# Kernel optimization log

Measured on AMD Instinct MI355X. Metric: run time of the kernel, lower is better.

## Reference

```python
import jax, jax.numpy as jnp
import numpy as np

C = 512
CI = C // 4  # inter_channels
EPS = 1e-5


def _conv1x1(x, w, b):
    # x: [B,C,H,W], w: [O,C], b: [O] -> [B,O,H,W]
    return jnp.einsum('bchw,oc->bohw', x, w) + b[None, :, None, None]


def _maxpool2(t):
    # 2x2 max pool, stride 2 (NCHW)
    b, c, h, w = t.shape
    return t.reshape(b, c, h // 2, 2, w // 2, 2).max(axis=(3, 5))


def setup_inputs() -> dict:
    key = jax.random.key(0)
    ks = jax.random.split(key, 9)
    B, H, W = 8, 64, 64
    s_in = 1.0 / np.sqrt(C)
    s_ci = 1.0 / np.sqrt(CI)
    return {
        'x': jax.random.normal(ks[0], (B, C, H, W), jnp.float32),
        'g_w': jax.random.normal(ks[1], (CI, C), jnp.float32) * s_in,
        'g_b': jnp.zeros((CI,), jnp.float32),
        'phi_w': jax.random.normal(ks[2], (CI, C), jnp.float32) * s_in,
        'phi_b': jnp.zeros((CI,), jnp.float32),
        'theta_w': jax.random.normal(ks[3], (CI, C), jnp.float32) * s_in,
        'theta_b': jnp.zeros((CI,), jnp.float32),
        'W_w': jax.random.normal(ks[4], (C, CI), jnp.float32) * s_ci,
        'W_b': jnp.zeros((C,), jnp.float32),
        'ln_gamma': jax.random.normal(ks[5], (C,), jnp.float32) * 0.02 + 1.0,
        'ln_beta': jnp.zeros((C,), jnp.float32),
    }


def reference(x, g_w, g_b, phi_w, phi_b, theta_w, theta_b, W_w, W_b, ln_gamma, ln_beta):
    B, Cc, H, Wd = x.shape
    N = H * Wd
    # projections; g and phi are maxpool-downsampled (N/4 key/value positions)
    g_x = _maxpool2(_conv1x1(x, g_w, g_b)).reshape(B, CI, N // 4)          # [B,Ci,M]
    phi_x = _maxpool2(_conv1x1(x, phi_w, phi_b)).reshape(B, CI, N // 4)    # [B,Ci,M]
    theta_x = _conv1x1(x, theta_w, theta_b).reshape(B, CI, N)              # [B,Ci,N]
    # attention: QK^T -> softmax -> V
    f = jnp.einsum('bcn,bcm->bnm', theta_x, phi_x)                          # [B,N,M]
    attn = jax.nn.softmax(f, axis=-1)
    y = jnp.einsum('bnm,bcm->bcn', attn, g_x).reshape(B, CI, H, Wd)         # [B,Ci,H,W]
    # output projection + channels-first LayerNorm + residual
    W_y = _conv1x1(y, W_w, W_b)                                             # [B,C,H,W]
    mu = W_y.mean(axis=1, keepdims=True)
    var = W_y.var(axis=1, keepdims=True)
    W_y = (W_y - mu) * jax.lax.rsqrt(var + EPS)
    W_y = W_y * ln_gamma[None, :, None, None] + ln_beta[None, :, None, None]
    return W_y + x
```

## Files before the change

kernel.cpp:

```cpp
#include <hip/hip_runtime.h>
#include <math.h>

constexpr int Cc  = 512;
constexpr int CIc = 128;
constexpr int Bc  = 8;
constexpr int Nc  = 4096;
constexpr int Mc  = 1024;

typedef __bf16 bf16x8 __attribute__((ext_vector_type(8)));
typedef float  f32x4  __attribute__((ext_vector_type(4)));

__device__ __forceinline__ unsigned short f2bf(float f) {
  unsigned u = __float_as_uint(f);
  u += 0x7fffu + ((u >> 16) & 1u);
  return (unsigned short)(u >> 16);
}
__device__ __forceinline__ float bf2f(unsigned short h) {
  return __uint_as_float((unsigned)h << 16);
}
__device__ __forceinline__ unsigned pack2bf(float lo, float hi) {
  return (unsigned)f2bf(lo) | ((unsigned)f2bf(hi) << 16);
}

__device__ __forceinline__ void gload16(const void* g, void* lds) {
  __builtin_amdgcn_global_load_lds(
      (const __attribute__((address_space(1))) unsigned int*)g,
      (__attribute__((address_space(3))) unsigned int*)lds, 16, 0, 0);
}

__global__ __launch_bounds__(256) void k_prep(
    const float* __restrict__ gw, const float* __restrict__ pw,
    const float* __restrict__ tw, const float* __restrict__ Ww,
    const float* __restrict__ gb, const float* __restrict__ pb,
    const float* __restrict__ tb,
    unsigned short* __restrict__ wcat, unsigned short* __restrict__ wwb,
    float* __restrict__ bcat) {
  int i = blockIdx.x * 256 + threadIdx.x;
  if (i < 49152) {
    int c = i >> 7, q = i & 127;
    const float* src = (c < 128) ? tw + (size_t)c * 512
                     : (c < 256) ? pw + (size_t)(c - 128) * 512
                                 : gw + (size_t)(c - 256) * 512;
    float4 v = *(const float4*)(src + q * 4);
    ushort4 o;
    o.x = f2bf(v.x); o.y = f2bf(v.y); o.z = f2bf(v.z); o.w = f2bf(v.w);
    *(ushort4*)(wcat + (size_t)c * 512 + q * 4) = o;
  } else if (i < 65536) {
    int i2 = i - 49152;
    int c = i2 >> 5, q = i2 & 31;
    float4 v = *(const float4*)(Ww + (size_t)c * 128 + q * 4);
    ushort4 o;
    o.x = f2bf(v.x); o.y = f2bf(v.y); o.z = f2bf(v.z); o.w = f2bf(v.w);
    *(ushort4*)(wwb + (size_t)c * 128 + q * 4) = o;
  } else if (i < 65920) {
    int j = i - 65536;
    bcat[j] = (j < 128) ? tb[j] : (j < 256) ? pb[j - 128] : gb[j - 256];
  }
}

__global__ __launch_bounds__(512) void k_conv_all(
    const float* __restrict__ x, const unsigned short* __restrict__ wcat,
    const float* __restrict__ bcat,
    unsigned short* __restrict__ theta_t, unsigned short* __restrict__ phi_t,
    unsigned short* __restrict__ gbuf) {
  __shared__ __align__(16) char smem[98304];
  const int b = blockIdx.y, h2 = blockIdx.x, n0 = h2 * 128;
  const int t = threadIdx.x;
  const int w = t >> 6, l = t & 63, lr = l & 15, lg = l >> 4;

  const char* wsrc = (const char*)wcat;
  int woff[6];
#pragma unroll
  for (int i = 0; i < 6; ++i) {
    int r = (w * 6 + i) * 8 + (l >> 3);
    woff[i] = r * 1024 + (((l & 7) * 16) ^ ((r & 7) << 4));
  }

  const float* xb = x + (size_t)b * Cc * Nc + n0 + w * 16 + lr;

  float xraw[16];
#define LOADX(k0_)                                                        \
  {                                                                       \
    _Pragma("unroll")                                                     \
    for (int ks = 0; ks < 2; ++ks)                                        \
      _Pragma("unroll")                                                   \
      for (int j = 0; j < 8; ++j)                                         \
        xraw[ks * 8 + j] = xb[(size_t)((k0_) + ks * 32 + lg * 8 + j) * Nc]; \
  }
#define STAGEW(buf_, k0_)                                                 \
  {                                                                       \
    char* dst_ = smem + (buf_) * 49152;                                   \
    _Pragma("unroll")                                                     \
    for (int i = 0; i < 6; ++i)                                           \
      gload16(wsrc + (size_t)(k0_) * 2 + woff[i], dst_ + (w * 6 + i) * 1024); \
  }

  f32x4 acc[24];
#pragma unroll
  for (int tc = 0; tc < 24; ++tc) acc[tc] = (f32x4){0.f, 0.f, 0.f, 0.f};

  LOADX(0);
  STAGEW(0, 0);
  asm volatile("s_waitcnt vmcnt(0)" ::: "memory");
  __builtin_amdgcn_s_barrier();

  for (int c = 0; c < 8; ++c) {
    const int cur = c & 1;
    bf16x8 af[2];
#pragma unroll
    for (int ks = 0; ks < 2; ++ks) {
      union { unsigned u[4]; bf16x8 v; } ab;
#pragma unroll
      for (int q = 0; q < 4; ++q)
        ab.u[q] = pack2bf(xraw[ks * 8 + 2 * q], xraw[ks * 8 + 2 * q + 1]);
      af[ks] = ab.v;
    }
    if (c < 7) {
      LOADX((c + 1) * 64);
      STAGEW(cur ^ 1, (c + 1) * 64);
    }
    const char* Wb = smem + cur * 49152;
    __builtin_amdgcn_s_setprio(1);
#pragma unroll
    for (int ks = 0; ks < 2; ++ks)
#pragma unroll
      for (int tc = 0; tc < 24; ++tc) {
        int r = tc * 16 + lr;
        bf16x8 bfr = *(const bf16x8*)(
            Wb + r * 128 + ((lg * 16 + ks * 64) ^ ((lr & 7) << 4)));
        acc[tc] = __builtin_amdgcn_mfma_f32_16x16x32_bf16(af[ks], bfr, acc[tc], 0, 0, 0);
      }
    __builtin_amdgcn_s_setprio(0);
    asm volatile("s_waitcnt vmcnt(0)" ::: "memory");
    __builtin_amdgcn_s_barrier();
  }
#undef LOADX
#undef STAGEW

  unsigned short* PG = (unsigned short*)smem;
  unsigned short* Yt = (unsigned short*)(smem + 67584);
  const int rbase = w * 16 + lg * 4;

#pragma unroll
  for (int tc = 8; tc < 24; ++tc) {
    float bv = bcat[tc * 16 + lr];
#pragma unroll
    for (int reg = 0; reg < 4; ++reg)
      PG[(rbase + reg) * 264 + tc * 16 + lr - 128] = f2bf(acc[tc][reg] + bv);
  }
  if (w < 4) {
#pragma unroll
    for (int tc = 0; tc < 8; ++tc) {
      float bv = bcat[tc * 16 + lr];
#pragma unroll
      for (int reg = 0; reg < 4; ++reg)
        Yt[(rbase + reg) * 136 + tc * 16 + lr] = f2bf(acc[tc][reg] + bv);
    }
  }
  __syncthreads();
#pragma unroll
  for (int it = 0; it < 2; ++it) {
    int idx = it * 512 + t, n = idx >> 4, j = idx & 15;
    *(bf16x8*)(theta_t + (((size_t)(b * Nc + n0 + n)) << 7) + j * 8) =
        *(const bf16x8*)(Yt + n * 136 + j * 8);
  }
  {
    int mloc = t >> 4, j = t & 15;
    const unsigned short* r0 = &PG[(2 * mloc) * 264 + j * 8];
    const unsigned short* r1 = &PG[(2 * mloc + 1) * 264 + j * 8];
    const unsigned short* r2 = &PG[(64 + 2 * mloc) * 264 + j * 8];
    const unsigned short* r3 = &PG[(65 + 2 * mloc) * 264 + j * 8];
    unsigned short o[8];
#pragma unroll
    for (int q = 0; q < 8; ++q)
      o[q] = f2bf(fmaxf(fmaxf(bf2f(r0[q]), bf2f(r1[q])),
                        fmaxf(bf2f(r2[q]), bf2f(r3[q]))));
    unsigned short* dp = phi_t + (((size_t)(b * Mc + h2 * 32 + mloc)) << 7) + j * 8;
    *(ushort4*)dp = *(ushort4*)o;
    *(ushort4*)(dp + 4) = *(ushort4*)(o + 4);
  }
  {
    int ci = t >> 2, mq = t & 3;
    unsigned short tmp[8];
#pragma unroll
    for (int q = 0; q < 8; ++q) {
      int w2 = mq * 8 + q;
      float m0 = fmaxf(
          fmaxf(bf2f(PG[(2 * w2) * 264 + 128 + ci]),
                bf2f(PG[(2 * w2 + 1) * 264 + 128 + ci])),
          fmaxf(bf2f(PG[(64 + 2 * w2) * 264 + 128 + ci]),
                bf2f(PG[(65 + 2 * w2) * 264 + 128 + ci])));
      tmp[q] = f2bf(m0);
    }
    unsigned short* dst = gbuf + ((size_t)(b * CIc + ci)) * Mc + h2 * 32 + mq * 8;
    *(ushort4*)(dst) = *(ushort4*)(tmp);
    *(ushort4*)(dst + 4) = *(ushort4*)(tmp + 4);
  }
  __syncthreads();
  if (w >= 4) {
#pragma unroll
    for (int tc = 0; tc < 8; ++tc) {
      float bv = bcat[tc * 16 + lr];
#pragma unroll
      for (int reg = 0; reg < 4; ++reg)
        Yt[((w - 4) * 16 + lg * 4 + reg) * 136 + tc * 16 + lr] =
            f2bf(acc[tc][reg] + bv);
    }
  }
  __syncthreads();
#pragma unroll
  for (int it = 0; it < 2; ++it) {
    int idx = it * 512 + t, n = idx >> 4, j = idx & 15;
    *(bf16x8*)(theta_t + (((size_t)(b * Nc + n0 + 64 + n)) << 7) + j * 8) =
        *(const bf16x8*)(Yt + n * 136 + j * 8);
  }
}

__global__ __launch_bounds__(256) void k_attn_mfma(
    const unsigned short* __restrict__ theta_t,
    const unsigned short* __restrict__ phi_t,
    const unsigned short* __restrict__ gv,
    unsigned short* __restrict__ y_t) {
  __shared__ __align__(16) char Kb[2][16384];
  __shared__ __align__(16) char Vb[2][16384];
  __shared__ __align__(16) unsigned short Ps[4][16][72];
  const int b = blockIdx.y, n0 = blockIdx.x * 64;
  const int tid = threadIdx.x;
  const int w = tid >> 6, l = tid & 63;
  const int lr = l & 15, lg = l >> 4;

  const int krow_l = l >> 4, kchunk = (l & 15) * 16;
  const int vrow_l = l >> 3, vchunk = (l & 7) * 16;
  int koff[4], voff[4];
#pragma unroll
  for (int i = 0; i < 4; ++i) {
    int kr = w * 16 + i * 4 + krow_l;
    koff[i] = kr * 256 + (kchunk ^ ((kr & 7) << 4));
    int vr = w * 32 + i * 8 + vrow_l;
    voff[i] = vr * 2048 + (vchunk ^ ((vr & 7) << 4));
  }
  const char* kbase = (const char*)(phi_t + (((size_t)(b * Mc)) << 7));
  const char* vbase = (const char*)(gv + (((size_t)b) << 17));

  auto stage = [&](int buf, int t) {
#pragma unroll
    for (int i = 0; i < 4; ++i)
      gload16(kbase + t * 16384 + koff[i], &Kb[buf][(w * 4 + i) * 1024]);
#pragma unroll
    for (int i = 0; i < 4; ++i)
      gload16(vbase + t * 128 + voff[i], &Vb[buf][(w * 4 + i) * 1024]);
  };

  bf16x8 qf[4];
  {
    const unsigned short* qp =
        theta_t + (((size_t)(b * Nc + n0 + w * 16 + lr)) << 7);
#pragma unroll
    for (int kk = 0; kk < 4; ++kk)
      qf[kk] = *(const bf16x8*)(qp + kk * 32 + lg * 8);
  }
  f32x4 of[8];
#pragma unroll
  for (int ct = 0; ct < 8; ++ct) of[ct] = (f32x4){0.f, 0.f, 0.f, 0.f};
  float run_m[4], run_l[4];
#pragma unroll
  for (int r = 0; r < 4; ++r) { run_m[r] = -1e30f; run_l[r] = 0.f; }

  stage(0, 0);
  asm volatile("s_waitcnt vmcnt(0)" ::: "memory");
  __builtin_amdgcn_s_barrier();

  for (int t = 0; t < Mc / 64; ++t) {
    const int cur = t & 1;
    if (t + 1 < Mc / 64) stage(cur ^ 1, t + 1);
    const char* Ks = Kb[cur];
    const char* Vs = Vb[cur];
    f32x4 sm[4];
    __builtin_amdgcn_s_setprio(1);
#pragma unroll
    for (int mt = 0; mt < 4; ++mt) {
      f32x4 s = (f32x4){0.f, 0.f, 0.f, 0.f};
#pragma unroll
      for (int kk = 0; kk < 4; ++kk) {
        bf16x8 kf = *(const bf16x8*)(
            Ks + (mt * 16 + lr) * 256 + ((kk * 64 + lg * 16) ^ ((lr & 7) << 4)));
        s = __builtin_amdgcn_mfma_f32_16x16x32_bf16(qf[kk], kf, s, 0, 0, 0);
      }
      sm[mt] = s;
    }
    __builtin_amdgcn_s_setprio(0);
    float pmax[4];
#pragma unroll
    for (int reg = 0; reg < 4; ++reg) {
      float mx = fmaxf(fmaxf(sm[0][reg], sm[1][reg]), fmaxf(sm[2][reg], sm[3][reg]));
      mx = fmaxf(mx, __shfl_xor(mx, 1));
      mx = fmaxf(mx, __shfl_xor(mx, 2));
      mx = fmaxf(mx, __shfl_xor(mx, 4));
      mx = fmaxf(mx, __shfl_xor(mx, 8));
      pmax[reg] = mx;
    }
    bool need = (pmax[0] > run_m[0] + 8.f) | (pmax[1] > run_m[1] + 8.f) |
                (pmax[2] > run_m[2] + 8.f) | (pmax[3] > run_m[3] + 8.f);
    if (__any(need)) {
#pragma unroll
      for (int reg = 0; reg < 4; ++reg) {
        float nm = fmaxf(run_m[reg], pmax[reg]);
        float sc = __expf(run_m[reg] - nm);
        run_m[reg] = nm;
        run_l[reg] *= sc;
#pragma unroll
        for (int ct = 0; ct < 8; ++ct) of[ct][reg] *= sc;
      }
    }
#pragma unroll
    for (int reg = 0; reg < 4; ++reg) {
      float p0 = __expf(sm[0][reg] - run_m[reg]);
      float p1 = __expf(sm[1][reg] - run_m[reg]);
      float p2 = __expf(sm[2][reg] - run_m[reg]);
      float p3 = __expf(sm[3][reg] - run_m[reg]);
      unsigned pk01, pk23;
      asm("v_cvt_pk_bf16_f32 %0, %1, %2" : "=v"(pk01) : "v"(p0), "v"(p1));
      asm("v_cvt_pk_bf16_f32 %0, %1, %2" : "=v"(pk23) : "v"(p2), "v"(p3));
      unsigned short* pr = &Ps[w][lg * 4 + reg][lr];
      pr[0]  = (unsigned short)pk01;
      pr[16] = (unsigned short)(pk01 >> 16);
      pr[32] = (unsigned short)pk23;
      pr[48] = (unsigned short)(pk23 >> 16);
      float rs = (p0 + p1) + (p2 + p3);
      rs += __shfl_xor(rs, 1);
      rs += __shfl_xor(rs, 2);
      rs += __shfl_xor(rs, 4);
      rs += __shfl_xor(rs, 8);
      run_l[reg] += rs;
    }
    bf16x8 pa0 = *(const bf16x8*)(&Ps[w][lr][lg * 8]);
    bf16x8 pa1 = *(const bf16x8*)(&Ps[w][lr][32 + lg * 8]);
    __builtin_amdgcn_s_setprio(1);
#pragma unroll
    for (int ct = 0; ct < 8; ++ct) {
      bf16x8 vf0 = *(const bf16x8*)(
          Vs + (ct * 16 + lr) * 128 + ((lg * 16) ^ ((lr & 7) << 4)));
      of[ct] = __builtin_amdgcn_mfma_f32_16x16x32_bf16(pa0, vf0, of[ct], 0, 0, 0);
      bf16x8 vf1 = *(const bf16x8*)(
          Vs + (ct * 16 + lr) * 128 + ((64 + lg * 16) ^ ((lr & 7) << 4)));
      of[ct] = __builtin_amdgcn_mfma_f32_16x16x32_bf16(pa1, vf1, of[ct], 0, 0, 0);
    }
    __builtin_amdgcn_s_setprio(0);
    asm volatile("s_waitcnt vmcnt(0)" ::: "memory");
    __builtin_amdgcn_s_barrier();
  }
  float invl[4];
#pragma unroll
  for (int reg = 0; reg < 4; ++reg) invl[reg] = 1.f / run_l[reg];
  unsigned short* Ys = (unsigned short*)Kb;
#pragma unroll
  for (int ct = 0; ct < 8; ++ct)
#pragma unroll
    for (int reg = 0; reg < 4; ++reg)
      Ys[(w * 16 + lg * 4 + reg) * 128 + ct * 16 + lr] =
          f2bf(of[ct][reg] * invl[reg]);
  __syncthreads();
#pragma unroll
  for (int it = 0; it < 4; ++it) {
    int i = it * 256 + tid;
    int r = i >> 4, cl = i & 15;
    *(bf16x8*)(y_t + (((size_t)(b * Nc + n0 + r)) << 7) + cl * 8) =
        *(const bf16x8*)(Ys + r * 128 + cl * 8);
  }
}

__global__ __launch_bounds__(256) void k_wconv_mfma(
    const unsigned short* __restrict__ y_t, const unsigned short* __restrict__ wwb,
    const float* __restrict__ wbias, const float* __restrict__ gamma,
    const float* __restrict__ beta, const float* __restrict__ x,
    float* __restrict__ out) {
  __shared__ __align__(16) char smem[36864];
  unsigned short* WTs = (unsigned short*)smem;
  float* Ys = (float*)smem;
  const int b = blockIdx.y, n0 = blockIdx.x * 64;
  const int t = threadIdx.x;
  const int w = t >> 6, l = t & 63, lr = l & 15, lg = l >> 4;

  bf16x8 qf[4];
  {
    const unsigned short* qp = y_t + (((size_t)(b * Nc + n0 + w * 16 + lr)) << 7);
#pragma unroll
    for (int kk = 0; kk < 4; ++kk)
      qf[kk] = *(const bf16x8*)(qp + kk * 32 + lg * 8);
  }
  f32x4 acc[32];
#pragma unroll
  for (int i = 0; i < 32; ++i) acc[i] = (f32x4){0.f, 0.f, 0.f, 0.f};

#pragma unroll
  for (int cc = 0; cc < 4; ++cc) {
    __syncthreads();
#pragma unroll
    for (int it = 0; it < 8; ++it) {
      int i = it * 256 + t;
      int r = i >> 4, j = i & 15;
      bf16x8 v = *(const bf16x8*)(wwb + (((size_t)(cc * 128 + r)) << 7) + j * 8);
      *(bf16x8*)((char*)WTs + r * 256 + ((j * 16) ^ ((r & 7) << 4))) = v;
    }
    __syncthreads();
#pragma unroll
    for (int tc = 0; tc < 8; ++tc) {
      f32x4 a = acc[cc * 8 + tc];
      int r = tc * 16 + lr;
#pragma unroll
      for (int kk = 0; kk < 4; ++kk) {
        bf16x8 kf = *(const bf16x8*)(
            (char*)WTs + r * 256 + ((kk * 64 + lg * 16) ^ ((lr & 7) << 4)));
        a = __builtin_amdgcn_mfma_f32_16x16x32_bf16(qf[kk], kf, a, 0, 0, 0);
      }
      acc[cc * 8 + tc] = a;
    }
  }
  float s[4] = {0.f, 0.f, 0.f, 0.f}, q[4] = {0.f, 0.f, 0.f, 0.f};
#pragma unroll
  for (int cc = 0; cc < 4; ++cc)
#pragma unroll
    for (int tc = 0; tc < 8; ++tc) {
      float wb = wbias[cc * 128 + tc * 16 + lr];
      f32x4 a = acc[cc * 8 + tc];
#pragma unroll
      for (int reg = 0; reg < 4; ++reg) {
        a[reg] += wb;
        s[reg] += a[reg];
        q[reg] += a[reg] * a[reg];
      }
      acc[cc * 8 + tc] = a;
    }
  float mu[4], rs[4];
#pragma unroll
  for (int reg = 0; reg < 4; ++reg) {
    float sv = s[reg], qv = q[reg];
    sv += __shfl_xor(sv, 1); qv += __shfl_xor(qv, 1);
    sv += __shfl_xor(sv, 2); qv += __shfl_xor(qv, 2);
    sv += __shfl_xor(sv, 4); qv += __shfl_xor(qv, 4);
    sv += __shfl_xor(sv, 8); qv += __shfl_xor(qv, 8);
    mu[reg] = sv * (1.f / 512.f);
    float var = qv * (1.f / 512.f) - mu[reg] * mu[reg];
    rs[reg] = rsqrtf(var + 1e-5f);
  }
#pragma unroll
  for (int cc = 0; cc < 4; ++cc) {
    __syncthreads();
#pragma unroll
    for (int tc = 0; tc < 8; ++tc) {
      int c = cc * 128 + tc * 16 + lr;
      float ga = gamma[c], be = beta[c];
#pragma unroll
      for (int reg = 0; reg < 4; ++reg)
        Ys[(tc * 16 + lr) * 72 + w * 16 + lg * 4 + reg] =
            (acc[cc * 8 + tc][reg] - mu[reg]) * rs[reg] * ga + be;
    }
    __syncthreads();
#pragma unroll
    for (int it = 0; it < 8; ++it) {
      int idx = it * 256 + t;
      int r = idx >> 4, j = idx & 15;
      float4 v = *(const float4*)&Ys[r * 72 + j * 4];
      size_t gaddr = ((size_t)b * Cc + cc * 128 + r) * Nc + n0 + j * 4;
      float4 xv = *(const float4*)&x[gaddr];
      float4 o;
      o.x = v.x + xv.x; o.y = v.y + xv.y; o.z = v.z + xv.z; o.w = v.w + xv.w;
      *(float4*)&out[gaddr] = o;
    }
  }
}

extern "C" void kernel_launch(void* const* d_in, const int* in_sizes, int n_in,
                              void* d_out, int out_size, void* d_ws, size_t ws_size,
                              hipStream_t stream) {
  const float* x       = (const float*)d_in[0];
  const float* g_w     = (const float*)d_in[1];
  const float* g_b     = (const float*)d_in[2];
  const float* phi_w   = (const float*)d_in[3];
  const float* phi_b   = (const float*)d_in[4];
  const float* theta_w = (const float*)d_in[5];
  const float* theta_b = (const float*)d_in[6];
  const float* W_w     = (const float*)d_in[7];
  const float* W_b     = (const float*)d_in[8];
  const float* ln_g    = (const float*)d_in[9];
  const float* ln_b    = (const float*)d_in[10];
  float* out = (float*)d_out;

  unsigned short* theta_t = (unsigned short*)d_ws;
  unsigned short* y_t     = theta_t + (size_t)Bc * Nc * CIc;
  unsigned short* phi_t   = y_t + (size_t)Bc * Nc * CIc;
  unsigned short* gbuf    = phi_t + (size_t)Bc * Mc * CIc;
  unsigned short* wcat    = gbuf + (size_t)Bc * Mc * CIc;
  unsigned short* wwb     = wcat + (size_t)384 * 512;
  float*          bcat    = (float*)(wwb + (size_t)512 * 128);

  k_prep<<<dim3(258), dim3(256), 0, stream>>>(
      g_w, phi_w, theta_w, W_w, g_b, phi_b, theta_b, wcat, wwb, bcat);
  k_conv_all<<<dim3(Nc / 128, Bc), dim3(512), 0, stream>>>(
      x, wcat, bcat, theta_t, phi_t, gbuf);
  k_attn_mfma<<<dim3(Nc / 64, Bc), dim3(256), 0, stream>>>(
      theta_t, phi_t, gbuf, y_t);
  k_wconv_mfma<<<dim3(Nc / 64, Bc), dim3(256), 0, stream>>>(
      y_t, wwb, W_b, ln_g, ln_b, x, out);
}
```

Measured before the change: 112.6 us.

## Process two query tiles per wave in attention kernel with 128-thread blocks

Restructures the flash-attention kernel so each wave handles 32 query rows (two 16-row subtiles) instead of 16, halving the waves per block to two. Each K and V fragment read from LDS now feeds two MFMAs, which halves LDS read traffic per FLOP and gives more independent MFMA chains. The cost is roughly double the accumulator registers per wave and fewer waves per block to hide latency, which could cut occupancy.

```diff
diff --git a/kernel.cpp b/kernel.cpp
--- a/kernel.cpp
+++ b/kernel.cpp
@@ -216,55 +216,59 @@
   }
 }
 
-__global__ __launch_bounds__(256) void k_attn_mfma(
+__global__ __launch_bounds__(128) void k_attn_mfma(
     const unsigned short* __restrict__ theta_t,
     const unsigned short* __restrict__ phi_t,
     const unsigned short* __restrict__ gv,
     unsigned short* __restrict__ y_t) {
   __shared__ __align__(16) char Kb[2][16384];
   __shared__ __align__(16) char Vb[2][16384];
-  __shared__ __align__(16) unsigned short Ps[4][16][72];
+  __shared__ __align__(16) unsigned short Ps[2][32][72];
   const int b = blockIdx.y, n0 = blockIdx.x * 64;
   const int tid = threadIdx.x;
   const int w = tid >> 6, l = tid & 63;
   const int lr = l & 15, lg = l >> 4;
 
-  const int krow_l = l >> 4, kchunk = (l & 15) * 16;
-  const int vrow_l = l >> 3, vchunk = (l & 7) * 16;
-  int koff[4], voff[4];
-#pragma unroll
-  for (int i = 0; i < 4; ++i) {
-    int kr = w * 16 + i * 4 + krow_l;
-    koff[i] = kr * 256 + (kchunk ^ ((kr & 7) << 4));
-    int vr = w * 32 + i * 8 + vrow_l;
-    voff[i] = vr * 2048 + (vchunk ^ ((vr & 7) << 4));
+  int koff[8], voff[8];
+#pragma unroll
+  for (int i = 0; i < 8; ++i) {
+    int c = w * 8 + i;
+    int kr = c * 4 + (l >> 4);
+    koff[i] = kr * 256 + (((l & 15) * 16) ^ ((kr & 7) << 4));
+    int vr = c * 8 + (l >> 3);
+    voff[i] = vr * 2048 + (((l & 7) * 16) ^ ((vr & 7) << 4));
   }
   const char* kbase = (const char*)(phi_t + (((size_t)(b * Mc)) << 7));
   const char* vbase = (const char*)(gv + (((size_t)b) << 17));
 
   auto stage = [&](int buf, int t) {
 #pragma unroll
-    for (int i = 0; i < 4; ++i)
-      gload16(kbase + t * 16384 + koff[i], &Kb[buf][(w * 4 + i) * 1024]);
-#pragma unroll
-    for (int i = 0; i < 4; ++i)
-      gload16(vbase + t * 128 + voff[i], &Vb[buf][(w * 4 + i) * 1024]);
+    for (int i = 0; i < 8; ++i)
+      gload16(kbase + t * 16384 + koff[i], &Kb[buf][(w * 8 + i) * 1024]);
+#pragma unroll
+    for (int i = 0; i < 8; ++i)
+      gload16(vbase + t * 128 + voff[i], &Vb[buf][(w * 8 + i) * 1024]);
   };
 
-  bf16x8 qf[4];
-  {
+  bf16x8 qf[2][4];
+#pragma unroll
+  for (int s = 0; s < 2; ++s) {
     const unsigned short* qp =
-        theta_t + (((size_t)(b * Nc + n0 + w * 16 + lr)) << 7);
+        theta_t + (((size_t)(b * Nc + n0 + w * 32 + s * 16 + lr)) << 7);
 #pragma unroll
     for (int kk = 0; kk < 4; ++kk)
-      qf[kk] = *(const bf16x8*)(qp + kk * 32 + lg * 8);
-  }
-  f32x4 of[8];
-#pragma unroll
-  for (int ct = 0; ct < 8; ++ct) of[ct] = (f32x4){0.f, 0.f, 0.f, 0.f};
-  float run_m[4], run_l[4];
-#pragma unroll
-  for (int r = 0; r < 4; ++r) { run_m[r] = -1e30f; run_l[r] = 0.f; }
+      qf[s][kk] = *(const bf16x8*)(qp + kk * 32 + lg * 8);
+  }
+  f32x4 of[2][8];
+#pragma unroll
+  for (int s = 0; s < 2; ++s)
+#pragma unroll
+    for (int ct = 0; ct < 8; ++ct) of[s][ct] = (f32x4){0.f, 0.f, 0.f, 0.f};
+  float run_m[2][4], run_l[2][4];
+#pragma unroll
+  for (int s = 0; s < 2; ++s)
+#pragma unroll
+    for (int r = 0; r < 4; ++r) { run_m[s][r] = -1e30f; run_l[s][r] = 0.f; }
 
   stage(0, 0);
   asm volatile("s_waitcnt vmcnt(0)" ::: "memory");
@@ -275,94 +279,116 @@
     if (t + 1 < Mc / 64) stage(cur ^ 1, t + 1);
     const char* Ks = Kb[cur];
     const char* Vs = Vb[cur];
-    f32x4 sm[4];
+    f32x4 sm[2][4];
     __builtin_amdgcn_s_setprio(1);
 #pragma unroll
     for (int mt = 0; mt < 4; ++mt) {
-      f32x4 s = (f32x4){0.f, 0.f, 0.f, 0.f};
+      f32x4 s0 = (f32x4){0.f, 0.f, 0.f, 0.f};
+      f32x4 s1 = (f32x4){0.f, 0.f, 0.f, 0.f};
 #pragma unroll
       for (int kk = 0; kk < 4; ++kk) {
         bf16x8 kf = *(const bf16x8*)(
             Ks + (mt * 16 + lr) * 256 + ((kk * 64 + lg * 16) ^ ((lr & 7) << 4)));
-        s = __builtin_amdgcn_mfma_f32_16x16x32_bf16(qf[kk], kf, s, 0, 0, 0);
+        s0 = __builtin_amdgcn_mfma_f32_16x16x32_bf16(qf[0][kk], kf, s0, 0, 0, 0);
+        s1 = __builtin_amdgcn_mfma_f32_16x16x32_bf16(qf[1][kk], kf, s1, 0, 0, 0);
       }
-      sm[mt] = s;
+      sm[0][mt] = s0;
+      sm[1][mt] = s1;
     }
     __builtin_amdgcn_s_setprio(0);
-    float pmax[4];
-#pragma unroll
-    for (int reg = 0; reg < 4; ++reg) {
-      float mx = fmaxf(fmaxf(sm[0][reg], sm[1][reg]), fmaxf(sm[2][reg], sm[3][reg]));
-      mx = fmaxf(mx, __shfl_xor(mx, 1));
-      mx = fmaxf(mx, __shfl_xor(mx, 2));
-      mx = fmaxf(mx, __shfl_xor(mx, 4));
-      mx = fmaxf(mx, __shfl_xor(mx, 8));
-      pmax[reg] = mx;
-    }
-    bool need = (pmax[0] > run_m[0] + 8.f) | (pmax[1] > run_m[1] + 8.f) |
-                (pmax[2] > run_m[2] + 8.f) | (pmax[3] > run_m[3] + 8.f);
+    float pmax[2][4];
+#pragma unroll
+    for (int s = 0; s < 2; ++s)
+#pragma unroll
+      for (int reg = 0; reg < 4; ++reg) {
+        float mx = fmaxf(fmaxf(sm[s][0][reg], sm[s][1][reg]),
+                         fmaxf(sm[s][2][reg], sm[s][3][reg]));
+        mx = fmaxf(mx, __shfl_xor(mx, 1));
+        mx = fmaxf(mx, __shfl_xor(mx, 2));
+        mx = fmaxf(mx, __shfl_xor(mx, 4));
+        mx = fmaxf(mx, __shfl_xor(mx, 8));
+        pmax[s][reg] = mx;
+      }
+    bool need = false;
+#pragma unroll
+    for (int s = 0; s < 2; ++s)
+#pragma unroll
+      for (int reg = 0; reg < 4; ++reg)
+        need |= (pmax[s][reg] > run_m[s][reg] + 8.f);
     if (__any(need)) {
 #pragma unroll
+      for (int s = 0; s < 2; ++s)
+#pragma unroll
+        for (int reg = 0; reg < 4; ++reg) {
+          float nm = fmaxf(run_m[s][reg], pmax[s][reg]);
+          float sc = __expf(run_m[s][reg] - nm);
+          run_m[s][reg] = nm;
+          run_l[s][reg] *= sc;
+#pragma unroll
+          for (int ct = 0; ct < 8; ++ct) of[s][ct][reg] *= sc;
+        }
+    }
+#pragma unroll
+    for (int s = 0; s < 2; ++s)
+#pragma unroll
       for (int reg = 0; reg < 4; ++reg) {
-        float nm = fmaxf(run_m[reg], pmax[reg]);
-        float sc = __expf(run_m[reg] - nm);
-        run_m[reg] = nm;
-        run_l[reg] *= sc;
-#pragma unroll
-        for (int ct = 0; ct < 8; ++ct) of[ct][reg] *= sc;
+        float p0 = __expf(sm[s][0][reg] - run_m[s][reg]);
+        float p1 = __expf(sm[s][1][reg] - run_m[s][reg]);
+        float p2 = __expf(sm[s][2][reg] - run_m[s][reg]);
+        float p3 = __expf(sm[s][3][reg] - run_m[s][reg]);
+        unsigned pk01, pk23;
+        asm("v_cvt_pk_bf16_f32 %0, %1, %2" : "=v"(pk01) : "v"(p0), "v"(p1));
+        asm("v_cvt_pk_bf16_f32 %0, %1, %2" : "=v"(pk23) : "v"(p2), "v"(p3));
+        unsigned short* pr = &Ps[w][s * 16 + lg * 4 + reg][lr];
+        pr[0]  = (unsigned short)pk01;
+        pr[16] = (unsigned short)(pk01 >> 16);
+        pr[32] = (unsigned short)pk23;
+        pr[48] = (unsigned short)(pk23 >> 16);
+        float rs = (p0 + p1) + (p2 + p3);
+        rs += __shfl_xor(rs, 1);
+        rs += __shfl_xor(rs, 2);
+        rs += __shfl_xor(rs, 4);
+        rs += __shfl_xor(rs, 8);
+        run_l[s][reg] += rs;
       }
-    }
-#pragma unroll
-    for (int reg = 0; reg < 4; ++reg) {
-      float p0 = __expf(sm[0][reg] - run_m[reg]);
-      float p1 = __expf(sm[1][reg] - run_m[reg]);
-      float p2 = __expf(sm[2][reg] - run_m[reg]);
-      float p3 = __expf(sm[3][reg] - run_m[reg]);
-      unsigned pk01, pk23;
-      asm("v_cvt_pk_bf16_f32 %0, %1, %2" : "=v"(pk01) : "v"(p0), "v"(p1));
-      asm("v_cvt_pk_bf16_f32 %0, %1, %2" : "=v"(pk23) : "v"(p2), "v"(p3));
-      unsigned short* pr = &Ps[w][lg * 4 + reg][lr];
-      pr[0]  = (unsigned short)pk01;
-      pr[16] = (unsigned short)(pk01 >> 16);
-      pr[32] = (unsigned short)pk23;
-      pr[48] = (unsigned short)(pk23 >> 16);
-      float rs = (p0 + p1) + (p2 + p3);
-      rs += __shfl_xor(rs, 1);
-      rs += __shfl_xor(rs, 2);
-      rs += __shfl_xor(rs, 4);
-      rs += __shfl_xor(rs, 8);
-      run_l[reg] += rs;
-    }
-    bf16x8 pa0 = *(const bf16x8*)(&Ps[w][lr][lg * 8]);
-    bf16x8 pa1 = *(const bf16x8*)(&Ps[w][lr][32 + lg * 8]);
+    bf16x8 pa00 = *(const bf16x8*)(&Ps[w][lr][lg * 8]);
+    bf16x8 pa01 = *(const bf16x8*)(&Ps[w][lr][32 + lg * 8]);
+    bf16x8 pa10 = *(const bf16x8*)(&Ps[w][16 + lr][lg * 8]);
+    bf16x8 pa11 = *(const bf16x8*)(&Ps[w][16 + lr][32 + lg * 8]);
     __builtin_amdgcn_s_setprio(1);
 #pragma unroll
     for (int ct = 0; ct < 8; ++ct) {
       bf16x8 vf0 = *(const bf16x8*)(
           Vs + (ct * 16 + lr) * 128 + ((lg * 16) ^ ((lr & 7) << 4)));
-      of[ct] = __builtin_amdgcn_mfma_f32_16x16x32_bf16(pa0, vf0, of[ct], 0, 0, 0);
+      of[0][ct] = __builtin_amdgcn_mfma_f32_16x16x32_bf16(pa00, vf0, of[0][ct], 0, 0, 0);
+      of[1][ct] = __builtin_amdgcn_mfma_f32_16x16x32_bf16(pa10, vf0, of[1][ct], 0, 0, 0);
       bf16x8 vf1 = *(const bf16x8*)(
           Vs + (ct * 16 + lr) * 128 + ((64 + lg * 16) ^ ((lr & 7) << 4)));
-      of[ct] = __builtin_amdgcn_mfma_f32_16x16x32_bf16(pa1, vf1, of[ct], 0, 0, 0);
+      of[0][ct] = __builtin_amdgcn_mfma_f32_16x16x32_bf16(pa01, vf1, of[0][ct], 0, 0, 0);
+      of[1][ct] = __builtin_amdgcn_mfma_f32_16x16x32_bf16(pa11, vf1, of[1][ct], 0, 0, 0);
     }
     __builtin_amdgcn_s_setprio(0);
     asm volatile("s_waitcnt vmcnt(0)" ::: "memory");
     __builtin_amdgcn_s_barrier();
   }
-  float invl[4];
-#pragma unroll
-  for (int reg = 0; reg < 4; ++reg) invl[reg] = 1.f / run_l[reg];
+  float invl[2][4];
+#pragma unroll
+  for (int s = 0; s < 2; ++s)
+#pragma unroll
+    for (int reg = 0; reg < 4; ++reg) invl[s][reg] = 1.f / run_l[s][reg];
   unsigned short* Ys = (unsigned short*)Kb;
 #pragma unroll
-  for (int ct = 0; ct < 8; ++ct)
-#pragma unroll
-    for (int reg = 0; reg < 4; ++reg)
-      Ys[(w * 16 + lg * 4 + reg) * 128 + ct * 16 + lr] =
-          f2bf(of[ct][reg] * invl[reg]);
+  for (int s = 0; s < 2; ++s)
+#pragma unroll
+    for (int ct = 0; ct < 8; ++ct)
+#pragma unroll
+      for (int reg = 0; reg < 4; ++reg)
+        Ys[(w * 32 + s * 16 + lg * 4 + reg) * 128 + ct * 16 + lr] =
+            f2bf(of[s][ct][reg] * invl[s][reg]);
   __syncthreads();
 #pragma unroll
-  for (int it = 0; it < 4; ++it) {
-    int i = it * 256 + tid;
+  for (int it = 0; it < 8; ++it) {
+    int i = it * 128 + tid;
     int r = i >> 4, cl = i & 15;
     *(bf16x8*)(y_t + (((size_t)(b * Nc + n0 + r)) << 7) + cl * 8) =
         *(const bf16x8*)(Ys + r * 128 + cl * 8);
@@ -498,7 +524,7 @@
       g_w, phi_w, theta_w, W_w, g_b, phi_b, theta_b, wcat, wwb, bcat);
   k_conv_all<<<dim3(Nc / 128, Bc), dim3(512), 0, stream>>>(
       x, wcat, bcat, theta_t, phi_t, gbuf);
-  k_attn_mfma<<<dim3(Nc / 64, Bc), dim3(256), 0, stream>>>(
+  k_attn_mfma<<<dim3(Nc / 64, Bc), dim3(128), 0, stream>>>(
       theta_t, phi_t, gbuf, y_t);
   k_wconv_mfma<<<dim3(Nc / 64, Bc), dim3(256), 0, stream>>>(
       y_t, wwb, W_b, ln_g, ln_b, x, out);
```

After: 123.3 us. 9.5% more time.

## Double-buffer W weight tiles via direct global-to-LDS loads in output conv

Applied to the files above, without the earlier changes.

The output 1x1 conv kernel now stages each 128-row chunk of the W weights into one of two 32KB LDS buffers using direct global-to-LDS loads (gload16). The next chunk is prefetched while MFMAs run on the current one, replacing the register round-trip and two syncthreads per chunk. It also raises wave priority around the MFMA loop. LDS use grows from 36KB to 64KB per block, which may reduce occupancy.

```diff
diff --git a/kernel.cpp b/kernel.cpp
--- a/kernel.cpp
+++ b/kernel.cpp
@@ -374,13 +374,27 @@
     const float* __restrict__ wbias, const float* __restrict__ gamma,
     const float* __restrict__ beta, const float* __restrict__ x,
     float* __restrict__ out) {
-  __shared__ __align__(16) char smem[36864];
-  unsigned short* WTs = (unsigned short*)smem;
+  __shared__ __align__(16) char smem[65536];
   float* Ys = (float*)smem;
   const int b = blockIdx.y, n0 = blockIdx.x * 64;
   const int t = threadIdx.x;
   const int w = t >> 6, l = t & 63, lr = l & 15, lg = l >> 4;
 
+  int woff[8];
+#pragma unroll
+  for (int i = 0; i < 8; ++i) {
+    int r = (w * 8 + i) * 4 + (l >> 4);
+    woff[i] = r * 256 + ((((l & 15) * 16)) ^ ((r & 7) << 4));
+  }
+  const char* wbase = (const char*)wwb;
+
+  auto stageW = [&](int buf, int cc) {
+#pragma unroll
+    for (int i = 0; i < 8; ++i)
+      gload16(wbase + cc * 32768 + woff[i],
+              smem + buf * 32768 + (w * 8 + i) * 1024);
+  };
+
   bf16x8 qf[4];
   {
     const unsigned short* qp = y_t + (((size_t)(b * Nc + n0 + w * 16 + lr)) << 7);
@@ -392,17 +406,16 @@
 #pragma unroll
   for (int i = 0; i < 32; ++i) acc[i] = (f32x4){0.f, 0.f, 0.f, 0.f};
 
+  stageW(0, 0);
+  asm volatile("s_waitcnt vmcnt(0)" ::: "memory");
+  __builtin_amdgcn_s_barrier();
+
 #pragma unroll
   for (int cc = 0; cc < 4; ++cc) {
-    __syncthreads();
-#pragma unroll
-    for (int it = 0; it < 8; ++it) {
-      int i = it * 256 + t;
-      int r = i >> 4, j = i & 15;
-      bf16x8 v = *(const bf16x8*)(wwb + (((size_t)(cc * 128 + r)) << 7) + j * 8);
-      *(bf16x8*)((char*)WTs + r * 256 + ((j * 16) ^ ((r & 7) << 4))) = v;
-    }
-    __syncthreads();
+    const int cur = cc & 1;
+    if (cc < 3) stageW(cur ^ 1, cc + 1);
+    const char* WTs = smem + cur * 32768;
+    __builtin_amdgcn_s_setprio(1);
 #pragma unroll
     for (int tc = 0; tc < 8; ++tc) {
       f32x4 a = acc[cc * 8 + tc];
@@ -410,12 +423,16 @@
 #pragma unroll
       for (int kk = 0; kk < 4; ++kk) {
         bf16x8 kf = *(const bf16x8*)(
-            (char*)WTs + r * 256 + ((kk * 64 + lg * 16) ^ ((lr & 7) << 4)));
+            WTs + r * 256 + ((kk * 64 + lg * 16) ^ ((lr & 7) << 4)));
         a = __builtin_amdgcn_mfma_f32_16x16x32_bf16(qf[kk], kf, a, 0, 0, 0);
       }
       acc[cc * 8 + tc] = a;
     }
-  }
+    __builtin_amdgcn_s_setprio(0);
+    asm volatile("s_waitcnt vmcnt(0)" ::: "memory");
+    __builtin_amdgcn_s_barrier();
+  }
+
   float s[4] = {0.f, 0.f, 0.f, 0.f}, q[4] = {0.f, 0.f, 0.f, 0.f};
 #pragma unroll
   for (int cc = 0; cc < 4; ++cc)
```

New measurement: 111.4 us. About the same (-1.1%).
